# Kernel tuning notes

Hardware: AMD Instinct MI355X
Metric: run time of the kernel (lower is better)

Reference implementation:

```python
import jax, jax.numpy as jnp
import numpy as np

BS, SL, D, NH = 2, 2048, 1024, 16
HD = D // NH
SCALE = D ** (-0.5)  # NOTE: source scales by full model dim, not head dim


def setup_inputs() -> dict:
    key = jax.random.key(0)
    k1, k2, k3 = jax.random.split(key, 3)
    return {
        "input_sequence": jax.random.normal(k1, (BS, SL, D), dtype=jnp.float32),
        "w_qkv": jax.random.normal(k2, (D, 3 * D), dtype=jnp.float32) * (D ** -0.5),
        "w_out": jax.random.normal(k3, (D, D), dtype=jnp.float32) * (D ** -0.5),
    }


def reference(input_sequence, w_qkv, w_out):
    bs, sl, od = input_sequence.shape
    nh, hd = NH, od // NH
    qkv = input_sequence @ w_qkv                      # [bs, sl, 3d]
    q, k, v = jnp.split(qkv, 3, axis=-1)              # each [bs, sl, d]
    q = q * SCALE

    def heads(x):  # [bs, sl, d] -> [bs, nh, sl, hd]
        return x.reshape(bs, sl, nh, hd).transpose(0, 2, 1, 3)

    q, k, v = heads(q), heads(k), heads(v)
    scores = jnp.einsum("bhqd,bhkd->bhqk", q, k)      # [bs, nh, sl, sl]
    weights = jax.nn.softmax(scores, axis=-1)
    ctx = jnp.einsum("bhqk,bhkd->bhqd", weights, v)   # [bs, nh, sl, hd]
    ctx = ctx.transpose(0, 2, 1, 3).reshape(bs, sl, od)
    return ctx @ w_out
```

## Files before the change

kernel.cpp:

```cpp
#include <hip/hip_runtime.h>
#include <cstdint>
#include <cstddef>

typedef float f32x4 __attribute__((ext_vector_type(4)));
typedef float f32x16 __attribute__((ext_vector_type(16)));
typedef __bf16 bf16x8 __attribute__((ext_vector_type(8)));
typedef __bf16 bf16x4 __attribute__((ext_vector_type(4)));
typedef uint32_t u32x4 __attribute__((ext_vector_type(4)));

static constexpr int BSZ = 2, SL = 2048, DM = 1024, NH = 16, HD = 64;
static constexpr int MROWS = BSZ * SL;
static constexpr float LOG2E = 1.4426950408889634f;
static constexpr float QSCALE = 0.03125f * LOG2E;

__device__ __forceinline__ f32x4 mfma16(bf16x8 a, bf16x8 b, f32x4 c) {
    return __builtin_amdgcn_mfma_f32_16x16x32_bf16(a, b, c, 0, 0, 0);
}
__device__ __forceinline__ f32x16 mfma32(bf16x8 a, bf16x8 b, f32x16 c) {
    return __builtin_amdgcn_mfma_f32_32x32x16_bf16(a, b, c, 0, 0, 0);
}
__device__ __forceinline__ uint32_t pkbf(float lo, float hi) {
    uint16_t a = __builtin_bit_cast(uint16_t, (__bf16)lo);
    uint16_t b = __builtin_bit_cast(uint16_t, (__bf16)hi);
    return ((uint32_t)b << 16) | (uint32_t)a;
}
__device__ __forceinline__ float fexp2(float x) {
#if __has_builtin(__builtin_amdgcn_exp2f)
    return __builtin_amdgcn_exp2f(x);
#else
    float r; asm volatile("v_exp_f32 %0, %1" : "=v"(r) : "v"(x)); return r;
#endif
}
__device__ __forceinline__ void gload16(const void* g, void* l) {
    __builtin_amdgcn_global_load_lds(
        (const __attribute__((address_space(1))) uint32_t*)g,
        (__attribute__((address_space(3))) uint32_t*)l, 16, 0, 0);
}

__global__ __launch_bounds__(256) void r13_cast(const float* __restrict__ in,
                                                __bf16* __restrict__ out, int n) {
    int i = (blockIdx.x * 256 + threadIdx.x) * 4;
    if (i >= n) return;
    float4 v = *(const float4*)&in[i];
    bf16x4 o;
    o.x = (__bf16)v.x; o.y = (__bf16)v.y; o.z = (__bf16)v.z; o.w = (__bf16)v.w;
    *(bf16x4*)&out[i] = o;
}

__global__ __launch_bounds__(256) void r13_transpose_cast(const float* __restrict__ in,
                                                          __bf16* __restrict__ out,
                                                          int R, int C) {
    __shared__ float tile[32][33];
    int c0 = blockIdx.x * 32, r0 = blockIdx.y * 32;
    int tx = threadIdx.x & 31, ty = threadIdx.x >> 5;
#pragma unroll
    for (int i = 0; i < 32; i += 8)
        tile[ty + i][tx] = in[(size_t)(r0 + ty + i) * C + c0 + tx];
    __syncthreads();
#pragma unroll
    for (int i = 0; i < 32; i += 8)
        out[(size_t)(c0 + ty + i) * R + r0 + tx] = (__bf16)tile[tx][ty + i];
}

template <int EPI, int BN>
__global__ __launch_bounds__(256) void r13_gemm(
    const __bf16* __restrict__ A, const __bf16* __restrict__ Bt,
    float* __restrict__ ob, int M, int N, int K,
    __bf16* __restrict__ qb, __bf16* __restrict__ kb, __bf16* __restrict__ vtb)
{
    constexpr int BM = 128, BK = 32;
    constexpr int FN = BN / 32;
    __shared__ __bf16 As[BM * BK];
    __shared__ __bf16 Bs[BN * BK];
    const int tid  = threadIdx.x;
    const int m0   = blockIdx.y * BM, n0 = blockIdx.x * BN;
    const int wave = tid >> 6, lane = tid & 63;
    const int lcol = lane & 15, lgrp = lane >> 4;
    const int wm   = (wave >> 1) * 64, wn = (wave & 1) * (BN / 2);
    const int grow = lane >> 2, gcol = (lane & 3) * 8;

    f32x4 acc[4][FN] = {};

    for (int k0 = 0; k0 < K; k0 += BK) {
        {
            const int cA0 = 2 * wave;
            gload16(&A[(size_t)(m0 + cA0 * 16 + grow) * K + k0 + gcol], &As[cA0 * 512]);
            gload16(&A[(size_t)(m0 + (cA0 + 1) * 16 + grow) * K + k0 + gcol], &As[(cA0 + 1) * 512]);
            if constexpr (BN == 128) {
                gload16(&Bt[(size_t)(n0 + cA0 * 16 + grow) * K + k0 + gcol], &Bs[cA0 * 512]);
                gload16(&Bt[(size_t)(n0 + (cA0 + 1) * 16 + grow) * K + k0 + gcol], &Bs[(cA0 + 1) * 512]);
            } else {
                gload16(&Bt[(size_t)(n0 + wave * 16 + grow) * K + k0 + gcol], &Bs[wave * 512]);
            }
        }
        __syncthreads();
        bf16x8 af[4], bfr[FN];
#pragma unroll
        for (int f = 0; f < 4; ++f)
            af[f] = *(const bf16x8*)&As[(wm + f * 16 + lcol) * BK + lgrp * 8];
#pragma unroll
        for (int f = 0; f < FN; ++f)
            bfr[f] = *(const bf16x8*)&Bs[(wn + f * 16 + lcol) * BK + lgrp * 8];
#pragma unroll
        for (int fm = 0; fm < 4; ++fm)
#pragma unroll
            for (int fn = 0; fn < FN; ++fn)
                acc[fm][fn] = mfma16(af[fm], bfr[fn], acc[fm][fn]);
        __syncthreads();
    }

#pragma unroll
    for (int fm = 0; fm < 4; ++fm) {
#pragma unroll
        for (int fn = 0; fn < FN; ++fn) {
            int n = n0 + wn + fn * 16 + lcol;
#pragma unroll
            for (int r = 0; r < 4; ++r) {
                int m = m0 + wm + fm * 16 + lgrp * 4 + r;
                float v = acc[fm][fn][r];
                if (EPI == 0) {
                    ob[(size_t)m * N + n] = v;
                } else {
                    int sec = n >> 10, nm = n & 1023;
                    int h = nm >> 6, d = nm & 63;
                    int b = m >> 11, s = m & 2047;
                    size_t bh = (size_t)(b * NH + h);
                    if (sec == 0)      qb[(bh * SL + s) * HD + d]  = (__bf16)(v * QSCALE);
                    else if (sec == 1) kb[(bh * SL + s) * HD + d]  = (__bf16)v;
                    else               vtb[(bh * HD + d) * SL + s] = (__bf16)v;
                }
            }
        }
    }
}

#define PV2(PA, PB, O, KS) do {                                                 \
    uint32_t a0 = pkbf(PA[(O) + 0], PA[(O) + 1]);                               \
    uint32_t a1 = pkbf(PA[(O) + 2], PA[(O) + 3]);                               \
    uint32_t a2 = pkbf(PA[(O) + 4], PA[(O) + 5]);                               \
    uint32_t a3 = pkbf(PA[(O) + 6], PA[(O) + 7]);                               \
    asm volatile("v_permlane32_swap_b32 %0, %1" : "+v"(a0), "+v"(a2));          \
    asm volatile("v_permlane32_swap_b32 %0, %1" : "+v"(a1), "+v"(a3));          \
    u32x4 wa = {a0, a1, a2, a3};                                                \
    bf16x8 pfA = __builtin_bit_cast(bf16x8, wa);                                \
    uint32_t b0 = pkbf(PB[(O) + 0], PB[(O) + 1]);                               \
    uint32_t b1 = pkbf(PB[(O) + 2], PB[(O) + 3]);                               \
    uint32_t b2 = pkbf(PB[(O) + 4], PB[(O) + 5]);                               \
    uint32_t b3 = pkbf(PB[(O) + 6], PB[(O) + 7]);                               \
    asm volatile("v_permlane32_swap_b32 %0, %1" : "+v"(b0), "+v"(b2));          \
    asm volatile("v_permlane32_swap_b32 %0, %1" : "+v"(b1), "+v"(b3));          \
    u32x4 wb = {b0, b1, b2, b3};                                                \
    bf16x8 pfB = __builtin_bit_cast(bf16x8, wb);                                \
    const int cv = (((KS) * 2 + h) ^ swz8) * 8;                                 \
    bf16x8 vf0 = *(const bf16x8*)&Vl[lq * 64 + cv];                             \
    bf16x8 vf1 = *(const bf16x8*)&Vl[(lq + 32) * 64 + cv];                      \
    accT0 = mfma32(vf0, pfA, accT0);                                            \
    accT1 = mfma32(vf1, pfA, accT1);                                            \
    accT2 = mfma32(vf0, pfB, accT2);                                            \
    accT3 = mfma32(vf1, pfB, accT3);                                            \
} while (0)

#define TILE_BODY(TI, KA, KB, VA, VB) do {                                      \
    const int cur = (TI) & 1;                                                   \
    {                                                                           \
        __bf16* dK = &arena[cur * 8192 + oA];                                   \
        __bf16* dV = dK + 4096;                                                 \
        *(int4*)dK = KA;  *(int4*)(dK + 2048) = KB;                             \
        *(int4*)dV = VA;  *(int4*)(dV + 2048) = VB;                             \
    }                                                                           \
    if ((TI) + 2 < NT) {                                                        \
        const __bf16* nK = KgA + (size_t)((TI) + 2) * 64 * HD;                  \
        const __bf16* nV = VgA + (size_t)((TI) + 2) * 64;                       \
        KA = *(const int4*)(nK);                                                \
        KB = *(const int4*)(nK + (size_t)32 * HD);                              \
        VA = *(const int4*)(nV);                                                \
        VB = *(const int4*)(nV + (size_t)32 * SL);                              \
    }                                                                           \
    asm volatile("s_waitcnt lgkmcnt(0)" ::: "memory");                          \
    __builtin_amdgcn_s_barrier();                                               \
    __builtin_amdgcn_sched_barrier(0);                                          \
    const __bf16* Kl = &arena[cur * 8192];                                      \
    const __bf16* Vl = Kl + 4096;                                               \
    f32x16 sA0 = {}, sA1 = {}, sB0 = {}, sB1 = {};                              \
    __builtin_amdgcn_s_setprio(1);                                              \
    _Pragma("unroll")                                                           \
    for (int t4 = 0; t4 < 4; ++t4) {                                            \
        const int cv = ((t4 * 2 + h) ^ swz8) * 8;                               \
        bf16x8 kf0 = *(const bf16x8*)&Kl[lq * 64 + cv];                         \
        bf16x8 kf1 = *(const bf16x8*)&Kl[(lq + 32) * 64 + cv];                  \
        sA0 = mfma32(kf0, qfA[t4], sA0);                                        \
        sB0 = mfma32(kf0, qfB[t4], sB0);                                        \
        sA1 = mfma32(kf1, qfA[t4], sA1);                                        \
        sB1 = mfma32(kf1, qfB[t4], sB1);                                        \
    }                                                                           \
    __builtin_amdgcn_s_setprio(0);                                              \
    float pA0[16], pA1[16], pB0[16], pB1[16];                                   \
    _Pragma("unroll")                                                           \
    for (int i = 0; i < 16; ++i) {                                              \
        pA0[i] = fexp2(sA0[i]); pA1[i] = fexp2(sA1[i]);                         \
        pB0[i] = fexp2(sB0[i]); pB1[i] = fexp2(sB1[i]);                         \
    }                                                                           \
    __builtin_amdgcn_s_setprio(1);                                              \
    PV2(pA0, pB0, 0, 0);                                                        \
    PV2(pA0, pB0, 8, 1);                                                        \
    PV2(pA1, pB1, 0, 2);                                                        \
    PV2(pA1, pB1, 8, 3);                                                        \
    __builtin_amdgcn_s_setprio(0);                                              \
    float a16[16], b16[16];                                                     \
    _Pragma("unroll")                                                           \
    for (int i = 0; i < 16; ++i) { a16[i] = pA0[i] + pA1[i]; b16[i] = pB0[i] + pB1[i]; } \
    _Pragma("unroll")                                                           \
    for (int i = 0; i < 8; ++i) { a16[i] += a16[i + 8]; b16[i] += b16[i + 8]; } \
    _Pragma("unroll")                                                           \
    for (int i = 0; i < 4; ++i) { a16[i] += a16[i + 4]; b16[i] += b16[i + 4]; } \
    float ltA = (a16[0] + a16[1]) + (a16[2] + a16[3]);                          \
    float ltB = (b16[0] + b16[1]) + (b16[2] + b16[3]);                          \
    ltA += __shfl_xor(ltA, 32);                                                 \
    ltB += __shfl_xor(ltB, 32);                                                 \
    lA += ltA;                                                                  \
    lB += ltB;                                                                  \
} while (0)

__global__ __launch_bounds__(256, 1) void r13_attn(
    const __bf16* __restrict__ qb, const __bf16* __restrict__ kb,
    const __bf16* __restrict__ vtb, __bf16* __restrict__ ctx)
{
    __shared__ __bf16 arena[16384];
    const int L = blockIdx.x + 8 * blockIdx.y;
    const int xcd = L & 7, j = L >> 3;
    const int bh = xcd * 4 + (j & 3);
    const int qblk = j >> 2;
    const int tid  = threadIdx.x;
    const int wave = tid >> 6, lane = tid & 63;
    const int lq = lane & 31, h = lane >> 5;
    const int swz8 = lq & 7;
    const int q0 = qblk * 256 + wave * 64;

    const __bf16* Q  = qb  + ((size_t)bh * SL + q0) * HD;
    const __bf16* Kg = kb  + (size_t)bh * SL * HD;
    const __bf16* Vg = vtb + (size_t)bh * HD * SL;

    const int rA = tid >> 3, cA = tid & 7;
    const int sA = cA ^ (rA & 7);
    const int oA = rA * 64 + sA * 8;

    bf16x8 qfA[4], qfB[4];
#pragma unroll
    for (int t = 0; t < 4; ++t) {
        qfA[t] = *(const bf16x8*)&Q[(size_t)lq * HD + t * 16 + h * 8];
        qfB[t] = *(const bf16x8*)&Q[(size_t)(lq + 32) * HD + t * 16 + h * 8];
    }

    f32x16 accT0 = {}, accT1 = {}, accT2 = {}, accT3 = {};
    float lA = 0.f, lB = 0.f;

    const __bf16* KgA = Kg + (size_t)rA * HD + cA * 8;
    const __bf16* VgA = Vg + (size_t)rA * SL + cA * 8;
    int4 kA0 = *(const int4*)(KgA);
    int4 kB0 = *(const int4*)(KgA + (size_t)32 * HD);
    int4 vA0 = *(const int4*)(VgA);
    int4 vB0 = *(const int4*)(VgA + (size_t)32 * SL);
    int4 kA1 = *(const int4*)(KgA + (size_t)64 * HD);
    int4 kB1 = *(const int4*)(KgA + (size_t)96 * HD);
    int4 vA1 = *(const int4*)(VgA + 64);
    int4 vB1 = *(const int4*)(VgA + (size_t)32 * SL + 64);

    constexpr int NT = SL / 64;
    for (int t = 0; t < NT; t += 2) {
        TILE_BODY(t,     kA0, kB0, vA0, vB0);
        TILE_BODY(t + 1, kA1, kB1, vA1, vB1);
    }

    float invA = 1.f / lA, invB = 1.f / lB;
    __syncthreads();
    __bf16* Osw = &arena[wave * 2304];
    const int b = bh >> 4, head = bh & 15;
    const int qr = lane >> 1, seg = (lane & 1) * 32;
#pragma unroll
    for (int r = 0; r < 16; ++r) {
        int d0 = (r & 3) + 8 * (r >> 2) + 4 * h;
        Osw[lq * 72 + d0]      = (__bf16)(accT0[r] * invA);
        Osw[lq * 72 + 32 + d0] = (__bf16)(accT1[r] * invA);
    }
    asm volatile("s_waitcnt lgkmcnt(0)" ::: "memory");
    __builtin_amdgcn_sched_barrier(0);
    {
        __bf16* dst = &ctx[((size_t)b * SL + q0 + qr) * DM + head * HD + seg];
#pragma unroll
        for (int c = 0; c < 4; ++c)
            *(bf16x8*)&dst[c * 8] = *(const bf16x8*)&Osw[qr * 72 + seg + c * 8];
    }
    asm volatile("s_waitcnt lgkmcnt(0)" ::: "memory");
    __builtin_amdgcn_sched_barrier(0);
#pragma unroll
    for (int r = 0; r < 16; ++r) {
        int d0 = (r & 3) + 8 * (r >> 2) + 4 * h;
        Osw[lq * 72 + d0]      = (__bf16)(accT2[r] * invB);
        Osw[lq * 72 + 32 + d0] = (__bf16)(accT3[r] * invB);
    }
    asm volatile("s_waitcnt lgkmcnt(0)" ::: "memory");
    __builtin_amdgcn_sched_barrier(0);
    {
        __bf16* dst = &ctx[((size_t)b * SL + q0 + 32 + qr) * DM + head * HD + seg];
#pragma unroll
        for (int c = 0; c < 4; ++c)
            *(bf16x8*)&dst[c * 8] = *(const bf16x8*)&Osw[qr * 72 + seg + c * 8];
    }
}

extern "C" void kernel_launch(void* const* d_in, const int* in_sizes, int n_in,
                              void* d_out, int out_size, void* d_ws, size_t ws_size,
                              hipStream_t stream) {
    const float* x    = (const float*)d_in[0];
    const float* wqkv = (const float*)d_in[1];
    const float* wout = (const float*)d_in[2];
    float* out = (float*)d_out;

    __bf16* ws    = (__bf16*)d_ws;
    __bf16* xb    = ws;
    __bf16* wqkvT = xb    + (size_t)MROWS * DM;
    __bf16* woutT = wqkvT + (size_t)3 * DM * DM;
    __bf16* qbuf  = woutT + (size_t)DM * DM;
    __bf16* kbuf  = qbuf  + (size_t)MROWS * DM;
    __bf16* vtbuf = kbuf  + (size_t)MROWS * DM;
    __bf16* ctxb  = vtbuf + (size_t)MROWS * DM;

    r13_cast<<<dim3((MROWS * DM) / 1024), dim3(256), 0, stream>>>(x, xb, MROWS * DM);
    r13_transpose_cast<<<dim3(96, 32), dim3(256), 0, stream>>>(wqkv, wqkvT, DM, 3 * DM);
    r13_transpose_cast<<<dim3(32, 32), dim3(256), 0, stream>>>(wout, woutT, DM, DM);

    r13_gemm<1, 128><<<dim3(24, 32), dim3(256), 0, stream>>>(
        xb, wqkvT, (float*)nullptr, MROWS, 3 * DM, DM, qbuf, kbuf, vtbuf);

    r13_attn<<<dim3(8, 32), dim3(256), 0, stream>>>(qbuf, kbuf, vtbuf, ctxb);

    r13_gemm<0, 64><<<dim3(16, 32), dim3(256), 0, stream>>>(
        ctxb, woutT, out, MROWS, DM, DM,
        (__bf16*)nullptr, (__bf16*)nullptr, (__bf16*)nullptr);
}
```

Before: 139.5 us.

## Split attention KV range in two and merge partial outputs

```diff
diff --git a/kernel.cpp b/kernel.cpp
--- a/kernel.cpp
+++ b/kernel.cpp
@@ -37,7 +37,7 @@
         (__attribute__((address_space(3))) uint32_t*)l, 16, 0, 0);
 }
 
-__global__ __launch_bounds__(256) void r13_cast(const float* __restrict__ in,
+__global__ __launch_bounds__(256) void r14_cast(const float* __restrict__ in,
                                                 __bf16* __restrict__ out, int n) {
     int i = (blockIdx.x * 256 + threadIdx.x) * 4;
     if (i >= n) return;
@@ -47,7 +47,7 @@
     *(bf16x4*)&out[i] = o;
 }
 
-__global__ __launch_bounds__(256) void r13_transpose_cast(const float* __restrict__ in,
+__global__ __launch_bounds__(256) void r14_transpose_cast(const float* __restrict__ in,
                                                           __bf16* __restrict__ out,
                                                           int R, int C) {
     __shared__ float tile[32][33];
@@ -63,7 +63,7 @@
 }
 
 template <int EPI, int BN>
-__global__ __launch_bounds__(256) void r13_gemm(
+__global__ __launch_bounds__(256) void r14_gemm(
     const __bf16* __restrict__ A, const __bf16* __restrict__ Bt,
     float* __restrict__ ob, int M, int N, int K,
     __bf16* __restrict__ qb, __bf16* __restrict__ kb, __bf16* __restrict__ vtb)
@@ -221,20 +221,23 @@
     lB += ltB;                                                                  \
 } while (0)
 
-__global__ __launch_bounds__(256, 1) void r13_attn(
+__global__ __launch_bounds__(256, 2) void r14_attn(
     const __bf16* __restrict__ qb, const __bf16* __restrict__ kb,
-    const __bf16* __restrict__ vtb, __bf16* __restrict__ ctx)
+    const __bf16* __restrict__ vtb, __bf16* __restrict__ part0,
+    __bf16* __restrict__ part1, float* __restrict__ lbuf)
 {
     __shared__ __bf16 arena[16384];
-    const int L = blockIdx.x + 8 * blockIdx.y;
+    const int L = blockIdx.x + 8 * (blockIdx.y + 32 * blockIdx.z);
     const int xcd = L & 7, j = L >> 3;
     const int bh = xcd * 4 + (j & 3);
-    const int qblk = j >> 2;
+    const int qblk  = (j >> 2) & 7;
+    const int split = j >> 5;
     const int tid  = threadIdx.x;
     const int wave = tid >> 6, lane = tid & 63;
     const int lq = lane & 31, h = lane >> 5;
     const int swz8 = lq & 7;
     const int q0 = qblk * 256 + wave * 64;
+    const int kv0 = split * (SL / 2);
 
     const __bf16* Q  = qb  + ((size_t)bh * SL + q0) * HD;
     const __bf16* Kg = kb  + (size_t)bh * SL * HD;
@@ -254,8 +257,8 @@
     f32x16 accT0 = {}, accT1 = {}, accT2 = {}, accT3 = {};
     float lA = 0.f, lB = 0.f;
 
-    const __bf16* KgA = Kg + (size_t)rA * HD + cA * 8;
-    const __bf16* VgA = Vg + (size_t)rA * SL + cA * 8;
+    const __bf16* KgA = Kg + (size_t)(kv0 + rA) * HD + cA * 8;
+    const __bf16* VgA = Vg + (size_t)rA * SL + kv0 + cA * 8;
     int4 kA0 = *(const int4*)(KgA);
     int4 kB0 = *(const int4*)(KgA + (size_t)32 * HD);
     int4 vA0 = *(const int4*)(VgA);
@@ -265,10 +268,16 @@
     int4 vA1 = *(const int4*)(VgA + 64);
     int4 vB1 = *(const int4*)(VgA + (size_t)32 * SL + 64);
 
-    constexpr int NT = SL / 64;
+    constexpr int NT = SL / 2 / 64;
     for (int t = 0; t < NT; t += 2) {
         TILE_BODY(t,     kA0, kB0, vA0, vB0);
         TILE_BODY(t + 1, kA1, kB1, vA1, vB1);
+    }
+
+    if (h == 0) {
+        float* lb = lbuf + split * (32 * SL) + bh * SL;
+        lb[q0 + lq]      = lA;
+        lb[q0 + 32 + lq] = lB;
     }
 
     float invA = 1.f / lA, invB = 1.f / lB;
@@ -276,6 +285,7 @@
     __bf16* Osw = &arena[wave * 2304];
     const int b = bh >> 4, head = bh & 15;
     const int qr = lane >> 1, seg = (lane & 1) * 32;
+    __bf16* pbase = split == 0 ? part0 : part1;
 #pragma unroll
     for (int r = 0; r < 16; ++r) {
         int d0 = (r & 3) + 8 * (r >> 2) + 4 * h;
@@ -285,7 +295,7 @@
     asm volatile("s_waitcnt lgkmcnt(0)" ::: "memory");
     __builtin_amdgcn_sched_barrier(0);
     {
-        __bf16* dst = &ctx[((size_t)b * SL + q0 + qr) * DM + head * HD + seg];
+        __bf16* dst = &pbase[((size_t)b * SL + q0 + qr) * DM + head * HD + seg];
 #pragma unroll
         for (int c = 0; c < 4; ++c)
             *(bf16x8*)&dst[c * 8] = *(const bf16x8*)&Osw[qr * 72 + seg + c * 8];
@@ -301,11 +311,32 @@
     asm volatile("s_waitcnt lgkmcnt(0)" ::: "memory");
     __builtin_amdgcn_sched_barrier(0);
     {
-        __bf16* dst = &ctx[((size_t)b * SL + q0 + 32 + qr) * DM + head * HD + seg];
+        __bf16* dst = &pbase[((size_t)b * SL + q0 + 32 + qr) * DM + head * HD + seg];
 #pragma unroll
         for (int c = 0; c < 4; ++c)
             *(bf16x8*)&dst[c * 8] = *(const bf16x8*)&Osw[qr * 72 + seg + c * 8];
     }
+}
+
+__global__ __launch_bounds__(256) void r14_merge(
+    const __bf16* __restrict__ p0, const __bf16* __restrict__ p1,
+    const float* __restrict__ lbuf, __bf16* __restrict__ out)
+{
+    int idx = blockIdx.x * 256 + threadIdx.x;
+    int m = idx >> 7, g = idx & 127;
+    int d0 = g * 8, hh = d0 >> 6;
+    int b = m >> 11, q = m & 2047;
+    int bhq = (b * NH + hh) * SL + q;
+    float l0 = lbuf[bhq], l1 = lbuf[32 * SL + bhq];
+    float inv = 1.f / (l0 + l1);
+    float w0 = l0 * inv, w1 = l1 * inv;
+    size_t off = (size_t)m * DM + d0;
+    bf16x8 a = *(const bf16x8*)&p0[off];
+    bf16x8 c = *(const bf16x8*)&p1[off];
+    bf16x8 o;
+#pragma unroll
+    for (int j = 0; j < 8; ++j) o[j] = (__bf16)(w0 * (float)a[j] + w1 * (float)c[j]);
+    *(bf16x8*)&out[off] = o;
 }
 
 extern "C" void kernel_launch(void* const* d_in, const int* in_sizes, int n_in,
@@ -324,17 +355,23 @@
     __bf16* kbuf  = qbuf  + (size_t)MROWS * DM;
     __bf16* vtbuf = kbuf  + (size_t)MROWS * DM;
     __bf16* ctxb  = vtbuf + (size_t)MROWS * DM;
-
-    r13_cast<<<dim3((MROWS * DM) / 1024), dim3(256), 0, stream>>>(x, xb, MROWS * DM);
-    r13_transpose_cast<<<dim3(96, 32), dim3(256), 0, stream>>>(wqkv, wqkvT, DM, 3 * DM);
-    r13_transpose_cast<<<dim3(32, 32), dim3(256), 0, stream>>>(wout, woutT, DM, DM);
-
-    r13_gemm<1, 128><<<dim3(24, 32), dim3(256), 0, stream>>>(
+    __bf16* part0 = xb;
+    __bf16* part1 = ctxb;
+    float*  lbuf  = (float*)wqkvT;
+
+    r14_cast<<<dim3((MROWS * DM) / 1024), dim3(256), 0, stream>>>(x, xb, MROWS * DM);
+    r14_transpose_cast<<<dim3(96, 32), dim3(256), 0, stream>>>(wqkv, wqkvT, DM, 3 * DM);
+    r14_transpose_cast<<<dim3(32, 32), dim3(256), 0, stream>>>(wout, woutT, DM, DM);
+
+    r14_gemm<1, 128><<<dim3(24, 32), dim3(256), 0, stream>>>(
         xb, wqkvT, (float*)nullptr, MROWS, 3 * DM, DM, qbuf, kbuf, vtbuf);
 
-    r13_attn<<<dim3(8, 32), dim3(256), 0, stream>>>(qbuf, kbuf, vtbuf, ctxb);
-
-    r13_gemm<0, 64><<<dim3(16, 32), dim3(256), 0, stream>>>(
+    r14_attn<<<dim3(8, 32, 2), dim3(256), 0, stream>>>(
+        qbuf, kbuf, vtbuf, part0, part1, lbuf);
+
+    r14_merge<<<dim3(2048), dim3(256), 0, stream>>>(part0, part1, lbuf, ctxb);
+
+    r14_gemm<0, 64><<<dim3(16, 32), dim3(256), 0, stream>>>(
         ctxb, woutT, out, MROWS, DM, DM,
         (__bf16*)nullptr, (__bf16*)nullptr, (__bf16*)nullptr);
 }
```

New measurement: 141.4 us. About the same (+1.3%).
